# Performance work log

Measured on AMD Instinct MI355X. Metric: run time of the kernel, lower is better.

The kernel has to match this reference:

```python
import jax, jax.numpy as jnp
import numpy as np

N, E, D = 100000, 1000000, 128  # nodes, edges, feature dim (in=hidden=out)
BN_EPS = 1e-5


def setup_inputs() -> dict:
    key = jax.random.key(0)
    ks = jax.random.split(key, 6)
    inp = {
        "x": jax.random.normal(ks[0], (N, D), dtype=jnp.float32),
        "edge_src": jax.random.randint(ks[1], (E,), 0, N),
        "edge_dst": jax.random.randint(ks[2], (E,), 0, N),
    }
    # GraphConv weights (xavier-ish) and biases for 3 layers
    for i in range(3):
        inp[f"W{i}"] = jax.random.normal(ks[3 + i], (D, D), dtype=jnp.float32) * np.float32(1.0 / np.sqrt(D))
        inp[f"b{i}"] = jnp.zeros((D,), dtype=jnp.float32)
    # BatchNorm (eval mode) params/buffers for the 2 inter-layer BNs
    for i in range(2):
        inp[f"bn_gamma{i}"] = jnp.ones((D,), dtype=jnp.float32)
        inp[f"bn_beta{i}"] = jnp.zeros((D,), dtype=jnp.float32)
        inp[f"bn_mean{i}"] = jnp.zeros((D,), dtype=jnp.float32)
        inp[f"bn_var{i}"] = jnp.ones((D,), dtype=jnp.float32)
    return inp


def _gcn_forward(x, edge_src, edge_dst, Ws, bs, bns):
    n = x.shape[0]
    ones = jnp.ones((edge_src.shape[0],), x.dtype)
    # DGL GraphConv norm='both': D_out^{-1/2} on source, D_in^{-1/2} on dest, degrees clamped to >=1
    deg_out = jnp.clip(jax.ops.segment_sum(ones, edge_src, num_segments=n), 1.0)
    deg_in = jnp.clip(jax.ops.segment_sum(ones, edge_dst, num_segments=n), 1.0)
    norm_src = deg_out ** -0.5
    norm_dst = deg_in ** -0.5
    h = x
    L = len(Ws)
    for i in range(L):
        hs = (h * norm_src[:, None]) @ Ws[i]                     # [N, D] dense transform first
        agg = jax.ops.segment_sum(hs[edge_src], edge_dst, num_segments=n)  # SpMM: gather + scatter-add
        h = agg * norm_dst[:, None] + bs[i]
        if i < L - 1:  # BN (eval) + activation between layers; dropout=0 -> no-op
            g, bta, m, v = bns[i]
            h = (h - m) * jax.lax.rsqrt(v + BN_EPS) * g + bta
            h = jax.nn.relu(h)
    return h


def reference(x, edge_src, edge_dst, W0, b0, W1, b1, W2, b2,
              bn_gamma0, bn_beta0, bn_mean0, bn_var0,
              bn_gamma1, bn_beta1, bn_mean1, bn_var1):
    Ws = (W0, W1, W2)
    bs = (b0, b1, b2)
    bns = ((bn_gamma0, bn_beta0, bn_mean0, bn_var0),
           (bn_gamma1, bn_beta1, bn_mean1, bn_var1))
    return _gcn_forward(x, edge_src, edge_dst, Ws, bs, bns)
```

## Files before the change

### kernel.cpp

```cpp
#include <hip/hip_runtime.h>
#include <hip/hip_fp16.h>
#include <math.h>

#define D 128
#define NSL 32
#define PBU 25088

typedef _Float16 half8 __attribute__((ext_vector_type(8)));
typedef float f32x4 __attribute__((ext_vector_type(4)));

__device__ inline uint pack_f16x2(float a, float b) {
  __half2 h = __floats2half2_rn(a, b);
  return *reinterpret_cast<uint*>(&h);
}
__device__ inline float2 unpack_f16x2(uint p) {
  __half2 h = *reinterpret_cast<__half2*>(&p);
  return __half22float2(h);
}
__device__ inline uint mdiv40(uint x, uint M) {
  return (uint)(((unsigned long long)x * M) >> 40);
}


__global__ __launch_bounds__(1024) void k_build1(const int* __restrict__ esrc,
                                                 const int* __restrict__ edst,
                                                 const float* __restrict__ W0,
                                                 const float* __restrict__ W1,
                                                 const float* __restrict__ W2,
                                                 const float* __restrict__ b0,
                                                 const float* __restrict__ b1,
                                                 const float* __restrict__ b2,
                                                 const float* __restrict__ g0,
                                                 const float* __restrict__ be0,
                                                 const float* __restrict__ mu0,
                                                 const float* __restrict__ vr0,
                                                 const float* __restrict__ g1,
                                                 const float* __restrict__ be1,
                                                 const float* __restrict__ mu1,
                                                 const float* __restrict__ vr1,
                                                 uint* __restrict__ pd,
                                                 uint* __restrict__ ps,
                                                 uchar* __restrict__ rank8,
                                                 ushort* __restrict__ Wt,
                                                 float* __restrict__ CA,
                                                 float* __restrict__ CB,
                                                 int E, int SB) {
  __shared__ uint h[PBU];
  const int b = blockIdx.x;
  const int t = threadIdx.x;
  if (b < 32) {
    for (int j = t; j < PBU; j += 1024) h[j] = 0u;
    __syncthreads();
    const int i0 = b * SB, i1 = min(i0 + SB, E);
    for (int i = i0 + t; i < i1; i += 1024) {
      const int d = edst[i];
      const uint sh = (uint)(d & 3) * 8u;
      const uint old = atomicAdd(&h[d >> 2], 1u << sh);
      rank8[i] = (uchar)((old >> sh) & 0xffu);
    }
    __syncthreads();
    uint* p = pd + (size_t)b * PBU;
    for (int j = t; j < PBU; j += 1024) p[j] = h[j];
  } else if (b < 64) {
    const int sl = b - 32;
    for (int j = t; j < PBU; j += 1024) h[j] = 0u;
    __syncthreads();
    const int i0 = sl * SB, i1 = min(i0 + SB, E);
    for (int i = i0 + t; i < i1; i += 1024) {
      const int s = esrc[i];
      atomicAdd(&h[s >> 2], 1u << ((uint)(s & 3) * 8u));
    }
    __syncthreads();
    uint* p = ps + (size_t)sl * PBU;
    for (int j = t; j < PBU; j += 1024) p[j] = h[j];
  } else if (b < 112) {
    const int li = (b - 64) * 1024 + t;
    const int l = li >> 14;
    const int i = li & 16383;
    const int n = i >> 7, k = i & 127;
    const float* W = (l == 0) ? W0 : ((l == 1) ? W1 : W2);
    Wt[li] = __half_as_ushort(__float2half_rn(W[k * D + n]));
  } else if (t < D) {
    const int c = t;
    float A0 = g0[c] * rsqrtf(vr0[c] + 1e-5f);
    CA[c] = A0;
    CB[c] = (b0[c] - mu0[c]) * A0 + be0[c];
    float A1 = g1[c] * rsqrtf(vr1[c] + 1e-5f);
    CA[D + c] = A1;
    CB[D + c] = (b1[c] - mu1[c]) * A1 + be1[c];
    CA[2 * D + c] = 1.f;
    CB[2 * D + c] = b2[c];
  }
}


__global__ __launch_bounds__(256) void k_build2s(uint* __restrict__ pd,
                                                 const uint* __restrict__ ps,
                                                 int* __restrict__ totd,
                                                 float* __restrict__ ns,
                                                 float* __restrict__ nd,
                                                 int* __restrict__ csum,
                                                 int* __restrict__ rofs,
                                                 int* __restrict__ ticket,
                                                 int N, int nch) {
  __shared__ int sd[256];
  __shared__ int lastf;
  const int t = threadIdx.x;
  const int j = blockIdx.x * 256 + t;
  const int n0 = j * 4;
  uint r0 = 0, r1 = 0, r2 = 0, r3 = 0;
  uint s0 = 0, s1 = 0, s2 = 0, s3 = 0;
#pragma unroll
  for (int sl = 0; sl < NSL; ++sl) {
    const uint v = pd[(size_t)sl * PBU + j];
    pd[(size_t)sl * PBU + j] = r0 | (r1 << 8) | (r2 << 16) | (r3 << 24);
    r0 += v & 0xffu; r1 += (v >> 8) & 0xffu; r2 += (v >> 16) & 0xffu; r3 += (v >> 24) & 0xffu;
    const uint w = ps[(size_t)sl * PBU + j];
    s0 += w & 0xffu; s1 += (w >> 8) & 0xffu; s2 += (w >> 16) & 0xffu; s3 += (w >> 24) & 0xffu;
  }
  const uint rr[4] = {r0, r1, r2, r3};
  const uint ss[4] = {s0, s1, s2, s3};
  int tot = 0;
#pragma unroll
  for (int k = 0; k < 4; ++k) {
    if (n0 + k < N) {
      totd[n0 + k] = (int)rr[k];
      nd[n0 + k] = rsqrtf((float)max(rr[k], 1u));
      ns[n0 + k] = rsqrtf((float)max(ss[k], 1u));
      tot += (int)rr[k];
    }
  }
  sd[t] = tot; __syncthreads();
  for (int off = 128; off > 0; off >>= 1) {
    if (t < off) sd[t] += sd[t + off];
    __syncthreads();
  }
  if (t == 0) {
    csum[blockIdx.x] = sd[0];
    __threadfence();
    lastf = (atomicAdd(ticket, 1) == nch - 1) ? 1 : 0;
  }
  __syncthreads();
  if (lastf && t < 64) {
    __threadfence();
    int run = 0;
    for (int b0 = 0; b0 < nch; b0 += 64) {
      const int idx = b0 + t;
      int v = (idx < nch) ? __hip_atomic_load(&csum[idx], __ATOMIC_RELAXED,
                                              __HIP_MEMORY_SCOPE_AGENT) : 0;
      int sc = v;
#pragma unroll
      for (int off = 1; off < 64; off <<= 1) {
        int u = __shfl_up(sc, off);
        if (t >= off) sc += u;
      }
      if (idx < nch) csum[idx] = run + sc - v;
      run += __shfl(sc, 63);
    }
    if (t == 0) rofs[N] = run;
  }
}


__global__ __launch_bounds__(256) void k_scan_final(const int* __restrict__ totd,
                                                    const int* __restrict__ csum,
                                                    int* __restrict__ rofs, int n) {
  __shared__ int sd[256];
  const int b = blockIdx.x, t = threadIdx.x;
  const int base = b * 1024 + t * 4;
  int v[4]; int s = 0;
#pragma unroll
  for (int i = 0; i < 4; ++i) { v[i] = (base + i < n) ? totd[base + i] : 0; s += v[i]; }
  sd[t] = s; __syncthreads();
  for (int off = 1; off < 256; off <<= 1) {
    int x = (t >= off) ? sd[t - off] : 0;
    __syncthreads();
    sd[t] += x;
    __syncthreads();
  }
  int o = sd[t] - s + csum[b];
#pragma unroll
  for (int i = 0; i < 4; ++i) {
    if (base + i < n) { rofs[base + i] = o; o += v[i]; }
  }
}


__global__ __launch_bounds__(256) void k_sg(const float* __restrict__ X,
                                            const ushort* __restrict__ Wt,
                                            const float* __restrict__ ns,
                                            ushort* __restrict__ out,
                                            const int* __restrict__ esrc,
                                            const int* __restrict__ edst,
                                            const uchar* __restrict__ rank8,
                                            const uint* __restrict__ pd,
                                            const int* __restrict__ rofs,
                                            int* __restrict__ csr,
                                            int M, int E, uint Msb, int GB) {
  if ((int)blockIdx.x >= GB) {
    const int i = ((int)blockIdx.x - GB) * 256 + threadIdx.x;
    if (i < E) {
      const int d = edst[i];
      const uint sl = mdiv40((uint)i, Msb);
      const uint pk = pd[(size_t)sl * PBU + (d >> 2)];
      const uint pfx = (pk >> ((uint)(d & 3) * 8u)) & 0xffu;
      csr[rofs[d] + (int)pfx + (int)rank8[i]] = esrc[i];
    }
    return;
  }
  const int lane = threadIdx.x & 63;
  const int wv = threadIdx.x >> 6;
  const int m0 = (blockIdx.x * 4 + wv) * 32;
  if (m0 >= M) return;
  const int lr = lane & 15;
  const int kg = (lane >> 4) * 8;

  half8 hf[2][4];
  const half8 hz = {};
#pragma unroll
  for (int mt = 0; mt < 2; ++mt) {
    const int row = m0 + mt * 16 + lr;
    if (row < M) {
      const float s = ns[row];
#pragma unroll
      for (int kt = 0; kt < 4; ++kt) {
        const float4 a = *reinterpret_cast<const float4*>(X + (size_t)row * D + kt * 32 + kg);
        const float4 b = *reinterpret_cast<const float4*>(X + (size_t)row * D + kt * 32 + kg + 4);
        half8 hv;
        hv[0] = (_Float16)(a.x * s); hv[1] = (_Float16)(a.y * s);
        hv[2] = (_Float16)(a.z * s); hv[3] = (_Float16)(a.w * s);
        hv[4] = (_Float16)(b.x * s); hv[5] = (_Float16)(b.y * s);
        hv[6] = (_Float16)(b.z * s); hv[7] = (_Float16)(b.w * s);
        hf[mt][kt] = hv;
      }
    } else {
#pragma unroll
      for (int kt = 0; kt < 4; ++kt) hf[mt][kt] = hz;
    }
  }

  f32x4 acc[8][2];
#pragma unroll
  for (int nt = 0; nt < 8; ++nt) { acc[nt][0] = (f32x4)(0.f); acc[nt][1] = (f32x4)(0.f); }

#pragma unroll
  for (int nt = 0; nt < 8; ++nt) {
    const ushort* wb = Wt + (size_t)(nt * 16 + lr) * D + kg;
#pragma unroll
    for (int kt = 0; kt < 4; ++kt) {
      half8 wf = *reinterpret_cast<const half8*>(wb + kt * 32);
      acc[nt][0] = __builtin_amdgcn_mfma_f32_16x16x32_f16(wf, hf[0][kt], acc[nt][0], 0, 0, 0);
      acc[nt][1] = __builtin_amdgcn_mfma_f32_16x16x32_f16(wf, hf[1][kt], acc[nt][1], 0, 0, 0);
    }
  }

  const int mo = lane & 15;
  const int no = (lane >> 4) * 4;
#pragma unroll
  for (int mt = 0; mt < 2; ++mt) {
    const int row = m0 + mt * 16 + mo;
    if (row < M) {
#pragma unroll
      for (int nt = 0; nt < 8; ++nt) {
        uint2 u;
        u.x = pack_f16x2(acc[nt][mt][0], acc[nt][mt][1]);
        u.y = pack_f16x2(acc[nt][mt][2], acc[nt][mt][3]);
        *reinterpret_cast<uint2*>(out + (size_t)row * D + nt * 16 + no) = u;
      }
    }
  }
}


__global__ __launch_bounds__(256) void k_spgm(const uint* __restrict__ hs,
                                              const int* __restrict__ csr,
                                              const int* __restrict__ rofs,
                                              const float* __restrict__ nd,
                                              const float* __restrict__ ns,
                                              const float* __restrict__ CA,
                                              const float* __restrict__ CB,
                                              const ushort* __restrict__ Wt,
                                              ushort* __restrict__ out, int N) {
  __shared__ ushort A[128 * 136];
  const int t = threadIdx.x;
  const int lane = t & 63;
  const int c16 = lane & 15;
  const int gb = lane & ~15;
  const int g = t >> 4;
  const int rbase = blockIdx.x * 128;

#pragma unroll 1
  for (int r = 0; r < 8; ++r) {
    const int rl = g + 16 * r;
    const int d = rbase + rl;
    uint4 uo = make_uint4(0u, 0u, 0u, 0u);
    if (d < N) {
      const int beg = rofs[d], end = rofs[d + 1];
      float acc[8];
#pragma unroll
      for (int j = 0; j < 8; ++j) acc[j] = 0.f;
      for (int eb = beg; eb < end; eb += 16) {
        const int len = min(16, end - eb);
        const int idx = csr[min(eb + c16, end - 1)];
#pragma unroll 1
        for (int j = 0; j < len; j += 4) {
          const int l1 = min(j + 1, len - 1), l2 = min(j + 2, len - 1), l3 = min(j + 3, len - 1);
          const int s0 = __shfl(idx, gb + j);
          const int s1 = __shfl(idx, gb + l1);
          const int s2 = __shfl(idx, gb + l2);
          const int s3 = __shfl(idx, gb + l3);
          const float w1 = (j + 1 < len) ? 1.f : 0.f;
          const float w2 = (j + 2 < len) ? 1.f : 0.f;
          const float w3 = (j + 3 < len) ? 1.f : 0.f;
          const uint4 v0 = *reinterpret_cast<const uint4*>(hs + (size_t)s0 * 64 + c16 * 4);
          const uint4 v1 = *reinterpret_cast<const uint4*>(hs + (size_t)s1 * 64 + c16 * 4);
          const uint4 v2 = *reinterpret_cast<const uint4*>(hs + (size_t)s2 * 64 + c16 * 4);
          const uint4 v3 = *reinterpret_cast<const uint4*>(hs + (size_t)s3 * 64 + c16 * 4);
#pragma unroll
          for (int q = 0; q < 4; ++q) {
            const float2 a0 = unpack_f16x2((&v0.x)[q]);
            const float2 a1 = unpack_f16x2((&v1.x)[q]);
            const float2 a2 = unpack_f16x2((&v2.x)[q]);
            const float2 a3 = unpack_f16x2((&v3.x)[q]);
            acc[q * 2]     += a0.x;
            acc[q * 2 + 1] += a0.y;
            acc[q * 2]     = fmaf(a1.x, w1, acc[q * 2]);
            acc[q * 2 + 1] = fmaf(a1.y, w1, acc[q * 2 + 1]);
            acc[q * 2]     = fmaf(a2.x, w2, acc[q * 2]);
            acc[q * 2 + 1] = fmaf(a2.y, w2, acc[q * 2 + 1]);
            acc[q * 2]     = fmaf(a3.x, w3, acc[q * 2]);
            acc[q * 2 + 1] = fmaf(a3.y, w3, acc[q * 2 + 1]);
          }
        }
      }
      const float ndv = nd[d];
      const float s = ns[d];
      const float4 ca0 = *reinterpret_cast<const float4*>(CA + c16 * 8);
      const float4 ca1 = *reinterpret_cast<const float4*>(CA + c16 * 8 + 4);
      const float4 cb0 = *reinterpret_cast<const float4*>(CB + c16 * 8);
      const float4 cb1 = *reinterpret_cast<const float4*>(CB + c16 * 8 + 4);
      float rv[8];
      rv[0] = acc[0] * ndv * ca0.x + cb0.x;
      rv[1] = acc[1] * ndv * ca0.y + cb0.y;
      rv[2] = acc[2] * ndv * ca0.z + cb0.z;
      rv[3] = acc[3] * ndv * ca0.w + cb0.w;
      rv[4] = acc[4] * ndv * ca1.x + cb1.x;
      rv[5] = acc[5] * ndv * ca1.y + cb1.y;
      rv[6] = acc[6] * ndv * ca1.z + cb1.z;
      rv[7] = acc[7] * ndv * ca1.w + cb1.w;
#pragma unroll
      for (int j = 0; j < 8; ++j) rv[j] = fmaxf(rv[j], 0.f) * s;
      uo.x = pack_f16x2(rv[0], rv[1]);
      uo.y = pack_f16x2(rv[2], rv[3]);
      uo.z = pack_f16x2(rv[4], rv[5]);
      uo.w = pack_f16x2(rv[6], rv[7]);
    }
    *reinterpret_cast<uint4*>(&A[rl * 136 + c16 * 8]) = uo;
  }
  __syncthreads();

  const int w = t >> 6;
  const int m0l = w * 32;
  const int m0 = rbase + m0l;
  if (m0 >= N) return;
  const int lr = lane & 15;
  const int kg = (lane >> 4) * 8;
  half8 hf[2][4];
#pragma unroll
  for (int mt = 0; mt < 2; ++mt) {
    const int row_l = m0l + mt * 16 + lr;
#pragma unroll
    for (int kt = 0; kt < 4; ++kt)
      hf[mt][kt] = *reinterpret_cast<const half8*>(&A[row_l * 136 + kt * 32 + kg]);
  }
  const int no = (lane >> 4) * 4;
#pragma unroll
  for (int nt = 0; nt < 8; ++nt) {
    f32x4 a0 = (f32x4)(0.f), a1 = (f32x4)(0.f);
    const ushort* wb = Wt + (size_t)(nt * 16 + lr) * D + kg;
#pragma unroll
    for (int kt = 0; kt < 4; ++kt) {
      half8 wf = *reinterpret_cast<const half8*>(wb + kt * 32);
      a0 = __builtin_amdgcn_mfma_f32_16x16x32_f16(wf, hf[0][kt], a0, 0, 0, 0);
      a1 = __builtin_amdgcn_mfma_f32_16x16x32_f16(wf, hf[1][kt], a1, 0, 0, 0);
    }
    const int r0 = m0 + lr, r1 = m0 + 16 + lr;
    if (r0 < N) {
      uint2 u; u.x = pack_f16x2(a0[0], a0[1]); u.y = pack_f16x2(a0[2], a0[3]);
      *reinterpret_cast<uint2*>(out + (size_t)r0 * D + nt * 16 + no) = u;
    }
    if (r1 < N) {
      uint2 u; u.x = pack_f16x2(a1[0], a1[1]); u.y = pack_f16x2(a1[2], a1[3]);
      *reinterpret_cast<uint2*>(out + (size_t)r1 * D + nt * 16 + no) = u;
    }
  }
}


__global__ __launch_bounds__(256) void k_spmm16(const uint* __restrict__ hs,
                                                const int* __restrict__ csr,
                                                const int* __restrict__ rofs,
                                                const float* __restrict__ nd,
                                                const float* __restrict__ CA,
                                                const float* __restrict__ CB,
                                                float* __restrict__ outf, int N) {
  const int t = threadIdx.x;
  const int lane = t & 63;
  const int c16 = lane & 15;
  const int gb = lane & ~15;
  const int d = blockIdx.x * 16 + (t >> 4);
  if (d >= N) return;
  const int beg = rofs[d], end = rofs[d + 1];

  float acc[8];
#pragma unroll
  for (int j = 0; j < 8; ++j) acc[j] = 0.f;

  for (int base = beg; base < end; base += 16) {
    const int len = min(16, end - base);
    const int idx = csr[min(base + c16, end - 1)];
#pragma unroll 1
    for (int j = 0; j < len; j += 4) {
      const int l1 = min(j + 1, len - 1), l2 = min(j + 2, len - 1), l3 = min(j + 3, len - 1);
      const int s0 = __shfl(idx, gb + j);
      const int s1 = __shfl(idx, gb + l1);
      const int s2 = __shfl(idx, gb + l2);
      const int s3 = __shfl(idx, gb + l3);
      const float w1 = (j + 1 < len) ? 1.f : 0.f;
      const float w2 = (j + 2 < len) ? 1.f : 0.f;
      const float w3 = (j + 3 < len) ? 1.f : 0.f;
      const uint4 v0 = *reinterpret_cast<const uint4*>(hs + (size_t)s0 * 64 + c16 * 4);
      const uint4 v1 = *reinterpret_cast<const uint4*>(hs + (size_t)s1 * 64 + c16 * 4);
      const uint4 v2 = *reinterpret_cast<const uint4*>(hs + (size_t)s2 * 64 + c16 * 4);
      const uint4 v3 = *reinterpret_cast<const uint4*>(hs + (size_t)s3 * 64 + c16 * 4);
#pragma unroll
      for (int q = 0; q < 4; ++q) {
        const float2 a0 = unpack_f16x2((&v0.x)[q]);
        const float2 a1 = unpack_f16x2((&v1.x)[q]);
        const float2 a2 = unpack_f16x2((&v2.x)[q]);
        const float2 a3 = unpack_f16x2((&v3.x)[q]);
        acc[q * 2]     += a0.x;
        acc[q * 2 + 1] += a0.y;
        acc[q * 2]     = fmaf(a1.x, w1, acc[q * 2]);
        acc[q * 2 + 1] = fmaf(a1.y, w1, acc[q * 2 + 1]);
        acc[q * 2]     = fmaf(a2.x, w2, acc[q * 2]);
        acc[q * 2 + 1] = fmaf(a2.y, w2, acc[q * 2 + 1]);
        acc[q * 2]     = fmaf(a3.x, w3, acc[q * 2]);
        acc[q * 2 + 1] = fmaf(a3.y, w3, acc[q * 2 + 1]);
      }
    }
  }

  const float ndv = nd[d];
  const float4 ca0 = *reinterpret_cast<const float4*>(CA + c16 * 8);
  const float4 ca1 = *reinterpret_cast<const float4*>(CA + c16 * 8 + 4);
  const float4 cb0 = *reinterpret_cast<const float4*>(CB + c16 * 8);
  const float4 cb1 = *reinterpret_cast<const float4*>(CB + c16 * 8 + 4);
  float4 o0, o1;
  o0.x = acc[0] * ndv * ca0.x + cb0.x;
  o0.y = acc[1] * ndv * ca0.y + cb0.y;
  o0.z = acc[2] * ndv * ca0.z + cb0.z;
  o0.w = acc[3] * ndv * ca0.w + cb0.w;
  o1.x = acc[4] * ndv * ca1.x + cb1.x;
  o1.y = acc[5] * ndv * ca1.y + cb1.y;
  o1.z = acc[6] * ndv * ca1.z + cb1.z;
  o1.w = acc[7] * ndv * ca1.w + cb1.w;
  *reinterpret_cast<float4*>(outf + (size_t)d * D + c16 * 8) = o0;
  *reinterpret_cast<float4*>(outf + (size_t)d * D + c16 * 8 + 4) = o1;
}


extern "C" void kernel_launch(void* const* d_in, const int* in_sizes, int n_in,
                              void* d_out, int out_size, void* d_ws, size_t ws_size,
                              hipStream_t stream) {
  const float* x = (const float*)d_in[0];
  const int* esrc = (const int*)d_in[1];
  const int* edst = (const int*)d_in[2];
  const float* W0 = (const float*)d_in[3];
  const float* b0 = (const float*)d_in[4];
  const float* W1 = (const float*)d_in[5];
  const float* b1 = (const float*)d_in[6];
  const float* W2 = (const float*)d_in[7];
  const float* b2 = (const float*)d_in[8];
  const float* g0 = (const float*)d_in[9];
  const float* be0 = (const float*)d_in[10];
  const float* m0 = (const float*)d_in[11];
  const float* v0 = (const float*)d_in[12];
  const float* g1 = (const float*)d_in[13];
  const float* be1 = (const float*)d_in[14];
  const float* m1 = (const float*)d_in[15];
  const float* v1 = (const float*)d_in[16];
  const int N = in_sizes[0] / D;
  const int E = in_sizes[1];

  const int SB = (E + NSL - 1) / NSL;
  const uint Msb = (uint)(((1ULL << 40) + (unsigned long long)SB - 1) / (unsigned long long)SB);

  char* p = (char*)d_ws;
  auto carve = [&](size_t bytes) {
    char* r = p;
    p += (bytes + 255) & ~(size_t)255;
    return (void*)r;
  };
  uint* hs16 = (uint*)carve((size_t)N * 64 * 4);
  ushort* Wt = (ushort*)carve((size_t)3 * D * D * 2);
  float* CA = (float*)carve((size_t)3 * D * 4);
  float* CB = (float*)carve((size_t)3 * D * 4);
  float* ns = (float*)carve((size_t)N * 4);
  float* nd = (float*)carve((size_t)N * 4);
  uint* pd = (uint*)carve((size_t)NSL * PBU * 4);
  uint* ps = (uint*)carve((size_t)NSL * PBU * 4);
  uchar* rank8 = (uchar*)carve((size_t)E);
  int* totd = (int*)carve((size_t)N * 4);
  int* rofs = (int*)carve((size_t)(N + 1) * 4);
  const int nch = (N + 1023) / 1024;
  int* csum = (int*)carve((size_t)nch * 4);
  int* ticket = (int*)carve(256);
  int* csr = (int*)carve((size_t)E * 4);
  uint* hsOut = (uint*)d_out;

  hipMemsetAsync(ticket, 0, 4, stream);
  k_build1<<<113, 1024, 0, stream>>>(esrc, edst, W0, W1, W2, b0, b1, b2,
                                     g0, be0, m0, v0, g1, be1, m1, v1,
                                     pd, ps, rank8, Wt, CA, CB, E, SB);
  k_build2s<<<nch, 256, 0, stream>>>(pd, ps, totd, ns, nd, csum, rofs, ticket, N, nch);
  k_scan_final<<<nch, 256, 0, stream>>>(totd, csum, rofs, N);

  const int gb = (N + 127) / 128;
  const int scb = (E + 255) / 256;
  const int fb = (N + 127) / 128;
  const int sb = (N + 15) / 16;
  k_sg<<<gb + scb, 256, 0, stream>>>(x, Wt, ns, (ushort*)hs16, esrc, edst, rank8, pd, rofs,
                                     csr, N, E, Msb, gb);
  k_spgm<<<fb, 256, 0, stream>>>(hs16, csr, rofs, nd, ns, CA, CB, Wt + 16384,
                                 (ushort*)hsOut, N);
  k_spgm<<<fb, 256, 0, stream>>>(hsOut, csr, rofs, nd, ns, CA + D, CB + D, Wt + 32768,
                                 (ushort*)hs16, N);
  k_spmm16<<<sb, 256, 0, stream>>>(hs16, csr, rofs, nd, CA + 2 * D, CB + 2 * D,
                                   (float*)d_out, N);
}
```

Baseline: 226.4 us.

## Relabel nodes sorted by in-degree to balance SpMM work across warps

```diff
diff --git a/kernel.cpp b/kernel.cpp
--- a/kernel.cpp
+++ b/kernel.cpp
@@ -138,7 +138,7 @@
   if (t == 0) {
     csum[blockIdx.x] = sd[0];
     __threadfence();
-    lastf = (atomicAdd(ticket, 1) == nch - 1) ? 1 : 0;
+    lastf = (atomicAdd(&ticket[0], 1) == nch - 1) ? 1 : 0;
   }
   __syncthreads();
   if (lastf && t < 64) {
@@ -162,10 +162,16 @@
 }
 
 
-__global__ __launch_bounds__(256) void k_scan_final(const int* __restrict__ totd,
-                                                    const int* __restrict__ csum,
-                                                    int* __restrict__ rofs, int n) {
+__global__ __launch_bounds__(256) void k_scan_final2(const int* __restrict__ totd,
+                                                     const int* __restrict__ csum,
+                                                     int* __restrict__ rofs,
+                                                     ushort* __restrict__ drank,
+                                                     uint* __restrict__ phist,
+                                                     int* __restrict__ ticket,
+                                                     int n, int nch) {
   __shared__ int sd[256];
+  __shared__ uint hist[64];
+  __shared__ int lastf;
   const int b = blockIdx.x, t = threadIdx.x;
   const int base = b * 1024 + t * 4;
   int v[4]; int s = 0;
@@ -183,12 +189,75 @@
   for (int i = 0; i < 4; ++i) {
     if (base + i < n) { rofs[base + i] = o; o += v[i]; }
   }
+  if (t < 64) hist[t] = 0u;
+  __syncthreads();
+  uint rk[4];
+#pragma unroll
+  for (int i = 0; i < 4; ++i) {
+    if (base + i < n) {
+      const int bin = min(v[i], 63);
+      rk[i] = atomicAdd(&hist[bin], 1u);
+    }
+  }
+#pragma unroll
+  for (int i = 0; i < 4; ++i)
+    if (base + i < n) drank[base + i] = (ushort)rk[i];
+  __syncthreads();
+  if (t < 64) phist[b * 64 + t] = hist[t];
+  if (t == 0) {
+    __threadfence();
+    lastf = (atomicAdd(&ticket[1], 1) == nch - 1) ? 1 : 0;
+  }
+  __syncthreads();
+  if (lastf && t < 64) {
+    __threadfence();
+    uint sumb = 0;
+    for (int blk = 0; blk < nch; ++blk)
+      sumb += __hip_atomic_load(&phist[blk * 64 + t], __ATOMIC_RELAXED,
+                                __HIP_MEMORY_SCOPE_AGENT);
+    uint sc = sumb;
+#pragma unroll
+    for (int off = 1; off < 64; off <<= 1) {
+      uint u = __shfl_up(sc, off);
+      if (t >= off) sc += u;
+    }
+    uint run = sc - sumb;
+    for (int blk = 0; blk < nch; ++blk) {
+      const uint vv = __hip_atomic_load(&phist[blk * 64 + t], __ATOMIC_RELAXED,
+                                        __HIP_MEMORY_SCOPE_AGENT);
+      phist[blk * 64 + t] = run;
+      run += vv;
+    }
+  }
+}
+
+
+__global__ void k_permscat(const int* __restrict__ totd, const ushort* __restrict__ drank,
+                           const uint* __restrict__ pbase, const float* __restrict__ ns,
+                           const float* __restrict__ nd, const int* __restrict__ rofs,
+                           int* __restrict__ perm, int* __restrict__ inv,
+                           float* __restrict__ nsS, float* __restrict__ ndS,
+                           int* __restrict__ begS, int* __restrict__ degS, int N) {
+  const int nIdx = blockIdx.x * 256 + threadIdx.x;
+  if (nIdx >= N) return;
+  const int deg = totd[nIdx];
+  const int bin = min(deg, 63);
+  const int blk = nIdx >> 10;
+  const int pos = (int)pbase[blk * 64 + bin] + (int)drank[nIdx];
+  perm[pos] = nIdx;
+  inv[nIdx] = pos;
+  nsS[pos] = ns[nIdx];
+  ndS[pos] = nd[nIdx];
+  begS[pos] = rofs[nIdx];
+  degS[pos] = deg;
 }
 
 
 __global__ __launch_bounds__(256) void k_sg(const float* __restrict__ X,
                                             const ushort* __restrict__ Wt,
-                                            const float* __restrict__ ns,
+                                            const float* __restrict__ nsS,
+                                            const int* __restrict__ perm,
+                                            const int* __restrict__ inv,
                                             ushort* __restrict__ out,
                                             const int* __restrict__ esrc,
                                             const int* __restrict__ edst,
@@ -204,7 +273,7 @@
       const uint sl = mdiv40((uint)i, Msb);
       const uint pk = pd[(size_t)sl * PBU + (d >> 2)];
       const uint pfx = (pk >> ((uint)(d & 3) * 8u)) & 0xffu;
-      csr[rofs[d] + (int)pfx + (int)rank8[i]] = esrc[i];
+      csr[rofs[d] + (int)pfx + (int)rank8[i]] = inv[esrc[i]];
     }
     return;
   }
@@ -221,11 +290,12 @@
   for (int mt = 0; mt < 2; ++mt) {
     const int row = m0 + mt * 16 + lr;
     if (row < M) {
-      const float s = ns[row];
+      const int orig = perm[row];
+      const float s = nsS[row];
 #pragma unroll
       for (int kt = 0; kt < 4; ++kt) {
-        const float4 a = *reinterpret_cast<const float4*>(X + (size_t)row * D + kt * 32 + kg);
-        const float4 b = *reinterpret_cast<const float4*>(X + (size_t)row * D + kt * 32 + kg + 4);
+        const float4 a = *reinterpret_cast<const float4*>(X + (size_t)orig * D + kt * 32 + kg);
+        const float4 b = *reinterpret_cast<const float4*>(X + (size_t)orig * D + kt * 32 + kg + 4);
         half8 hv;
         hv[0] = (_Float16)(a.x * s); hv[1] = (_Float16)(a.y * s);
         hv[2] = (_Float16)(a.z * s); hv[3] = (_Float16)(a.w * s);
@@ -274,9 +344,10 @@
 
 __global__ __launch_bounds__(256) void k_spgm(const uint* __restrict__ hs,
                                               const int* __restrict__ csr,
-                                              const int* __restrict__ rofs,
-                                              const float* __restrict__ nd,
-                                              const float* __restrict__ ns,
+                                              const int* __restrict__ begS,
+                                              const int* __restrict__ degS,
+                                              const float* __restrict__ ndS,
+                                              const float* __restrict__ nsS,
                                               const float* __restrict__ CA,
                                               const float* __restrict__ CB,
                                               const ushort* __restrict__ Wt,
@@ -291,11 +362,12 @@
 
 #pragma unroll 1
   for (int r = 0; r < 8; ++r) {
-    const int rl = g + 16 * r;
+    const int rl = r * 16 + g;
     const int d = rbase + rl;
     uint4 uo = make_uint4(0u, 0u, 0u, 0u);
     if (d < N) {
-      const int beg = rofs[d], end = rofs[d + 1];
+      const int beg = begS[d];
+      const int end = beg + degS[d];
       float acc[8];
 #pragma unroll
       for (int j = 0; j < 8; ++j) acc[j] = 0.f;
@@ -333,8 +405,8 @@
           }
         }
       }
-      const float ndv = nd[d];
-      const float s = ns[d];
+      const float ndv = ndS[d];
+      const float s = nsS[d];
       const float4 ca0 = *reinterpret_cast<const float4*>(CA + c16 * 8);
       const float4 ca1 = *reinterpret_cast<const float4*>(CA + c16 * 8 + 4);
       const float4 cb0 = *reinterpret_cast<const float4*>(CB + c16 * 8);
@@ -399,8 +471,10 @@
 
 __global__ __launch_bounds__(256) void k_spmm16(const uint* __restrict__ hs,
                                                 const int* __restrict__ csr,
-                                                const int* __restrict__ rofs,
-                                                const float* __restrict__ nd,
+                                                const int* __restrict__ begS,
+                                                const int* __restrict__ degS,
+                                                const float* __restrict__ ndS,
+                                                const int* __restrict__ perm,
                                                 const float* __restrict__ CA,
                                                 const float* __restrict__ CB,
                                                 float* __restrict__ outf, int N) {
@@ -410,7 +484,8 @@
   const int gb = lane & ~15;
   const int d = blockIdx.x * 16 + (t >> 4);
   if (d >= N) return;
-  const int beg = rofs[d], end = rofs[d + 1];
+  const int beg = begS[d];
+  const int end = beg + degS[d];
 
   float acc[8];
 #pragma unroll
@@ -451,7 +526,8 @@
     }
   }
 
-  const float ndv = nd[d];
+  const float ndv = ndS[d];
+  const int orig = perm[d];
   const float4 ca0 = *reinterpret_cast<const float4*>(CA + c16 * 8);
   const float4 ca1 = *reinterpret_cast<const float4*>(CA + c16 * 8 + 4);
   const float4 cb0 = *reinterpret_cast<const float4*>(CB + c16 * 8);
@@ -465,8 +541,8 @@
   o1.y = acc[5] * ndv * ca1.y + cb1.y;
   o1.z = acc[6] * ndv * ca1.z + cb1.z;
   o1.w = acc[7] * ndv * ca1.w + cb1.w;
-  *reinterpret_cast<float4*>(outf + (size_t)d * D + c16 * 8) = o0;
-  *reinterpret_cast<float4*>(outf + (size_t)d * D + c16 * 8 + 4) = o1;
+  *reinterpret_cast<float4*>(outf + (size_t)orig * D + c16 * 8) = o0;
+  *reinterpret_cast<float4*>(outf + (size_t)orig * D + c16 * 8 + 4) = o1;
 }
 
 
@@ -502,12 +578,14 @@
     p += (bytes + 255) & ~(size_t)255;
     return (void*)r;
   };
-  uint* hs16 = (uint*)carve((size_t)N * 64 * 4);
+  uint* hsA = (uint*)carve((size_t)N * 64 * 4);
   ushort* Wt = (ushort*)carve((size_t)3 * D * D * 2);
   float* CA = (float*)carve((size_t)3 * D * 4);
   float* CB = (float*)carve((size_t)3 * D * 4);
   float* ns = (float*)carve((size_t)N * 4);
   float* nd = (float*)carve((size_t)N * 4);
+  float* nsS = (float*)carve((size_t)N * 4);
+  float* ndS = (float*)carve((size_t)N * 4);
   uint* pd = (uint*)carve((size_t)NSL * PBU * 4);
   uint* ps = (uint*)carve((size_t)NSL * PBU * 4);
   uchar* rank8 = (uchar*)carve((size_t)E);
@@ -517,25 +595,33 @@
   int* csum = (int*)carve((size_t)nch * 4);
   int* ticket = (int*)carve(256);
   int* csr = (int*)carve((size_t)E * 4);
-  uint* hsOut = (uint*)d_out;
-
-  hipMemsetAsync(ticket, 0, 4, stream);
+  ushort* drank = (ushort*)carve((size_t)N * 2);
+  uint* phist = (uint*)carve((size_t)nch * 64 * 4);
+  int* perm = (int*)carve((size_t)N * 4);
+  int* inv = (int*)carve((size_t)N * 4);
+  int* begS = (int*)carve((size_t)N * 4);
+  int* degS = (int*)carve((size_t)N * 4);
+  uint* hsB = (uint*)d_out;
+
+  hipMemsetAsync(ticket, 0, 8, stream);
   k_build1<<<113, 1024, 0, stream>>>(esrc, edst, W0, W1, W2, b0, b1, b2,
                                      g0, be0, m0, v0, g1, be1, m1, v1,
                                      pd, ps, rank8, Wt, CA, CB, E, SB);
   k_build2s<<<nch, 256, 0, stream>>>(pd, ps, totd, ns, nd, csum, rofs, ticket, N, nch);
-  k_scan_final<<<nch, 256, 0, stream>>>(totd, csum, rofs, N);
+  k_scan_final2<<<nch, 256, 0, stream>>>(totd, csum, rofs, drank, phist, ticket, N, nch);
+  k_permscat<<<(N + 255) / 256, 256, 0, stream>>>(totd, drank, phist, ns, nd, rofs,
+                                                  perm, inv, nsS, ndS, begS, degS, N);
 
   const int gb = (N + 127) / 128;
   const int scb = (E + 255) / 256;
   const int fb = (N + 127) / 128;
   const int sb = (N + 15) / 16;
-  k_sg<<<gb + scb, 256, 0, stream>>>(x, Wt, ns, (ushort*)hs16, esrc, edst, rank8, pd, rofs,
-                                     csr, N, E, Msb, gb);
-  k_spgm<<<fb, 256, 0, stream>>>(hs16, csr, rofs, nd, ns, CA, CB, Wt + 16384,
-                                 (ushort*)hsOut, N);
-  k_spgm<<<fb, 256, 0, stream>>>(hsOut, csr, rofs, nd, ns, CA + D, CB + D, Wt + 32768,
-                                 (ushort*)hs16, N);
-  k_spmm16<<<sb, 256, 0, stream>>>(hs16, csr, rofs, nd, CA + 2 * D, CB + 2 * D,
+  k_sg<<<gb + scb, 256, 0, stream>>>(x, Wt, nsS, perm, inv, (ushort*)hsA, esrc, edst,
+                                     rank8, pd, rofs, csr, N, E, Msb, gb);
+  k_spgm<<<fb, 256, 0, stream>>>(hsA, csr, begS, degS, ndS, nsS, CA, CB, Wt + 16384,
+                                 (ushort*)hsB, N);
+  k_spgm<<<fb, 256, 0, stream>>>(hsB, csr, begS, degS, ndS, nsS, CA + D, CB + D,
+                                 Wt + 32768, (ushort*)hsA, N);
+  k_spmm16<<<sb, 256, 0, stream>>>(hsA, csr, begS, degS, ndS, perm, CA + 2 * D, CB + 2 * D,
                                    (float*)d_out, N);
 }
```

Result: slower. 283.0 us (+25.0%).

## Partition CSR scatter by edge slice and destination range with vectorized edge loads

Applied to the files above, without the earlier changes.

```diff
diff --git a/kernel.cpp b/kernel.cpp
--- a/kernel.cpp
+++ b/kernel.cpp
@@ -16,9 +16,6 @@
 __device__ inline float2 unpack_f16x2(uint p) {
   __half2 h = *reinterpret_cast<__half2*>(&p);
   return __half22float2(h);
-}
-__device__ inline uint mdiv40(uint x, uint M) {
-  return (uint)(((unsigned long long)x * M) >> 40);
 }
 
 
@@ -196,15 +193,40 @@
                                             const uint* __restrict__ pd,
                                             const int* __restrict__ rofs,
                                             int* __restrict__ csr,
-                                            int M, int E, uint Msb, int GB) {
+                                            int M, int E, int SB, int BPC, int GB) {
   if ((int)blockIdx.x >= GB) {
-    const int i = ((int)blockIdx.x - GB) * 256 + threadIdx.x;
-    if (i < E) {
-      const int d = edst[i];
-      const uint sl = mdiv40((uint)i, Msb);
-      const uint pk = pd[(size_t)sl * PBU + (d >> 2)];
-      const uint pfx = (pk >> ((uint)(d & 3) * 8u)) & 0xffu;
-      csr[rofs[d] + (int)pfx + (int)rank8[i]] = esrc[i];
+    const int bb = (int)blockIdx.x - GB;
+    const int sl = bb >> 3;
+    const int c = bb & 7;
+    const int c0 = c * BPC;
+    const int c1 = min(c0 + BPC, M);
+    const int i0 = sl * SB;
+    const int i1 = min(i0 + SB, E);
+    const uint* pdsl = pd + (size_t)sl * PBU;
+    for (int vi = (i0 >> 2) + threadIdx.x; vi < ((i1 + 3) >> 2); vi += 256) {
+      const int ib = vi << 2;
+      int dv[4], sv[4];
+      if (ib + 3 < i1) {
+        const int4 d4 = reinterpret_cast<const int4*>(edst)[vi];
+        const int4 s4 = reinterpret_cast<const int4*>(esrc)[vi];
+        dv[0] = d4.x; dv[1] = d4.y; dv[2] = d4.z; dv[3] = d4.w;
+        sv[0] = s4.x; sv[1] = s4.y; sv[2] = s4.z; sv[3] = s4.w;
+      } else {
+#pragma unroll
+        for (int k = 0; k < 4; ++k) {
+          dv[k] = (ib + k < i1) ? edst[ib + k] : -1;
+          sv[k] = (ib + k < i1) ? esrc[ib + k] : 0;
+        }
+      }
+#pragma unroll
+      for (int k = 0; k < 4; ++k) {
+        const int d = dv[k];
+        if (d >= c0 && d < c1) {
+          const uint pk = pdsl[d >> 2];
+          const uint pfx = (pk >> ((uint)(d & 3) * 8u)) & 0xffu;
+          csr[rofs[d] + (int)pfx + (int)rank8[ib + k]] = sv[k];
+        }
+      }
     }
     return;
   }
@@ -493,8 +515,8 @@
   const int N = in_sizes[0] / D;
   const int E = in_sizes[1];
 
-  const int SB = (E + NSL - 1) / NSL;
-  const uint Msb = (uint)(((1ULL << 40) + (unsigned long long)SB - 1) / (unsigned long long)SB);
+  const int SB = (((E + NSL - 1) / NSL) + 3) & ~3;
+  const int BPC = (N + 7) / 8;
 
   char* p = (char*)d_ws;
   auto carve = [&](size_t bytes) {
@@ -527,11 +549,10 @@
   k_scan_final<<<nch, 256, 0, stream>>>(totd, csum, rofs, N);
 
   const int gb = (N + 127) / 128;
-  const int scb = (E + 255) / 256;
   const int fb = (N + 127) / 128;
   const int sb = (N + 15) / 16;
-  k_sg<<<gb + scb, 256, 0, stream>>>(x, Wt, ns, (ushort*)hs16, esrc, edst, rank8, pd, rofs,
-                                     csr, N, E, Msb, gb);
+  k_sg<<<gb + 256, 256, 0, stream>>>(x, Wt, ns, (ushort*)hs16, esrc, edst, rank8, pd, rofs,
+                                     csr, N, E, SB, BPC, gb);
   k_spgm<<<fb, 256, 0, stream>>>(hs16, csr, rofs, nd, ns, CA, CB, Wt + 16384,
                                  (ushort*)hsOut, N);
   k_spgm<<<fb, 256, 0, stream>>>(hsOut, csr, rofs, nd, ns, CA + D, CB + D, Wt + 32768,
```

Result: slower. 260.1 us (+14.9%).
